# Performance work log

Measured on AMD Instinct MI355X. Metric: run time of the kernel, lower is better.

## Reference

```python
import jax, jax.numpy as jnp
import numpy as np

N = 50000      # nodes
E = 800000     # edges (avg degree 16)
IN = 128       # in_channels
HID = 32       # hidden_channels per head
HEADS = 4
OUT = 64       # out_channels (last layer, heads=1, concat=False)
ED = 32        # edge_dim
NEG_SLOPE = 0.2


def _gatv2_layer(x, src, dst, ea, Wl, bl, Wr, br, We, att, bias, concat):
    """PyG GATv2Conv: lin_l -> source (x_j), lin_r -> target (x_i),
    score = att . leaky_relu(x_i + x_j + lin_edge(edge_attr)), segment-softmax over dst,
    out = scatter_add(alpha * x_j) per head, then concat or mean heads, plus bias."""
    n = x.shape[0]
    H, C = att.shape
    xl = (x @ Wl + bl).reshape(-1, H, C)   # [N,H,C] source transform
    xr = (x @ Wr + br).reshape(-1, H, C)   # [N,H,C] target transform
    ee = (ea @ We).reshape(-1, H, C)       # [E,H,C] edge transform
    m = jax.nn.leaky_relu(xl[src] + xr[dst] + ee, NEG_SLOPE)  # [E,H,C]
    a = jnp.einsum('ehc,hc->eh', m, att)   # [E,H] attention logits
    amax = jax.ops.segment_max(a, dst, num_segments=n)        # [N,H]
    ex = jnp.exp(a - amax[dst])
    den = jax.ops.segment_sum(ex, dst, num_segments=n)        # [N,H]
    alpha = ex / (den[dst] + 1e-16)        # [E,H] segment softmax
    out = jax.ops.segment_sum(xl[src] * alpha[..., None], dst, num_segments=n)  # [N,H,C]
    out = out.reshape(n, H * C) if concat else out.mean(axis=1)
    return out + bias


def setup_inputs() -> dict:
    key = jax.random.key(0)
    ks = jax.random.split(key, 20)
    s = 0.05
    HC = HEADS * HID
    inp = {
        'x': jax.random.normal(ks[0], (N, IN), jnp.float32),
        'edge_index': jax.random.randint(ks[1], (2, E), 0, N, jnp.int32),
        'edge_attr': jax.random.normal(ks[2], (E, ED), jnp.float32),
        # layer 1: GATv2Conv(IN -> HID, heads=HEADS, concat=True, edge_dim=ED)
        'Wl1': jax.random.normal(ks[3], (IN, HC), jnp.float32) * s,
        'bl1': jnp.zeros((HC,), jnp.float32),
        'Wr1': jax.random.normal(ks[4], (IN, HC), jnp.float32) * s,
        'br1': jnp.zeros((HC,), jnp.float32),
        'We1': jax.random.normal(ks[5], (ED, HC), jnp.float32) * s,
        'att1': jax.random.normal(ks[6], (HEADS, HID), jnp.float32) * s,
        'bias1': jnp.zeros((HC,), jnp.float32),
        # layer 2: GATv2Conv(HC -> OUT, heads=1, concat=False, edge_dim=ED)
        'Wl2': jax.random.normal(ks[7], (HC, OUT), jnp.float32) * s,
        'bl2': jnp.zeros((OUT,), jnp.float32),
        'Wr2': jax.random.normal(ks[8], (HC, OUT), jnp.float32) * s,
        'br2': jnp.zeros((OUT,), jnp.float32),
        'We2': jax.random.normal(ks[9], (ED, OUT), jnp.float32) * s,
        'att2': jax.random.normal(ks[10], (1, OUT), jnp.float32) * s,
        'bias2': jnp.zeros((OUT,), jnp.float32),
    }
    return inp


def reference(x, edge_index, edge_attr, Wl1, bl1, Wr1, br1, We1, att1, bias1,
              Wl2, bl2, Wr2, br2, We2, att2, bias2):
    src, dst = edge_index[0], edge_index[1]
    h = _gatv2_layer(x, src, dst, edge_attr, Wl1, bl1, Wr1, br1, We1, att1, bias1, concat=True)
    h = jax.nn.elu(h)
    out = _gatv2_layer(h, src, dst, edge_attr, Wl2, bl2, Wr2, br2, We2, att2, bias2, concat=False)
    return out
```

## Files before the change

kernel.cpp:

```cpp
#include <hip/hip_runtime.h>
#include <stdint.h>

#define N_NODES 50000
#define N_EDGES 800000

struct Ptrs { const void* p[16]; int n[16]; };

typedef __attribute__((ext_vector_type(8))) short bf16x8;
typedef __attribute__((ext_vector_type(4))) float f32x4;

__device__ __forceinline__ float bf2f(unsigned short u){
  union { unsigned int i; float f; } v; v.i = ((unsigned int)u) << 16; return v.f;
}
__device__ __forceinline__ float lo16(unsigned int u){ union { unsigned int i; float f; } v; v.i = u << 16; return v.f; }
__device__ __forceinline__ float hi16(unsigned int u){ union { unsigned int i; float f; } v; v.i = u & 0xffff0000u; return v.f; }
__device__ __forceinline__ unsigned short f2bf(float f){
  if (!(f == f)) return 0;
  unsigned int x = __float_as_uint(f);
  unsigned int r = (x + 0x7fffu + ((x >> 16) & 1u)) >> 16;
  return (unsigned short)r;
}
__device__ __forceinline__ float fin(float v){
  if (!(v == v)) return 0.f;
  return fminf(fmaxf(v, -1e30f), 1e30f);
}
__device__ __forceinline__ float loadF(const void* p, int f32, size_t idx){
  return f32 ? ((const float*)p)[idx] : bf2f(((const unsigned short*)p)[idx]);
}

__device__ __forceinline__ void stageW(unsigned short* dst, const void* src, int n, int f32, int tid){
  if (f32) {
    for (int i = tid * 8; i < n; i += 2048) {
      float4 a = *(const float4*)((const float*)src + i);
      float4 b = *(const float4*)((const float*)src + i + 4);
      uint4 u;
      u.x = (unsigned)f2bf(a.x) | ((unsigned)f2bf(a.y) << 16);
      u.y = (unsigned)f2bf(a.z) | ((unsigned)f2bf(a.w) << 16);
      u.z = (unsigned)f2bf(b.x) | ((unsigned)f2bf(b.y) << 16);
      u.w = (unsigned)f2bf(b.z) | ((unsigned)f2bf(b.w) << 16);
      *(uint4*)(dst + i) = u;
    }
  } else {
    for (int i = tid * 8; i < n; i += 2048)
      *(uint4*)(dst + i) = *(const uint4*)((const unsigned short*)src + i);
  }
}

__global__ __launch_bounds__(256) void k_detect(Ptrs tl, int* __restrict__ flags)
{
  __shared__ int red[256];
  int b = blockIdx.x, t = threadIdx.x;
  const unsigned short* p = (const unsigned short*)tl.p[b];
  int n = tl.n[b]; if (n > 16384) n = 16384;
  int crazy = 0;
  for (int i = t; i < n; i += 256) {
    unsigned short u = p[i];
    if (u) {
      int ex = (u >> 7) & 0xFF;
      if (ex == 0xFF || ex < 0x60) crazy++;
    }
  }
  red[t] = crazy; __syncthreads();
  for (int off = 128; off; off >>= 1) { if (t < off) red[t] += red[t + off]; __syncthreads(); }
  if (t == 0) flags[b] = (red[0] * 10 > n) ? 1 : 0;
}

__global__ __launch_bounds__(256) void k_zero(int* __restrict__ p, int n)
{
  int i = blockIdx.x * 256 + threadIdx.x;
  if (i < n) p[i] = 0;
}

__global__ __launch_bounds__(256) void k_gemm1(
    const void* __restrict__ x,
    const void* __restrict__ Wl, const void* __restrict__ bl,
    const void* __restrict__ Wr, const void* __restrict__ br,
    const int* __restrict__ flags,
    unsigned int* __restrict__ xlp, unsigned int* __restrict__ xrp)
{
  __shared__ float xs[32 * 132];
  __shared__ unsigned short ws[128 * 128];
  const void* W  = blockIdx.y ? Wr : Wl;
  const void* bb = blockIdx.y ? br : bl;
  int fW = blockIdx.y ? flags[4] : flags[2];
  int fB = blockIdx.y ? flags[5] : flags[3];
  int fX = flags[0];
  unsigned int* outp = blockIdx.y ? xrp : xlp;
  int tid = threadIdx.x;
  int row0 = blockIdx.x * 32;
  stageW(ws, W, 128 * 128, fW, tid);
  for (int i = tid * 4; i < 32 * 128; i += 1024) {
    int r = i >> 7, k = i & 127;
    int row = row0 + r;
    float4 v = make_float4(0.f, 0.f, 0.f, 0.f);
    if (row < N_NODES) {
      if (fX) v = *(const float4*)((const float*)x + (size_t)row * 128 + k);
      else {
        uint2 u = *(const uint2*)((const unsigned short*)x + (size_t)row * 128 + k);
        v.x = lo16(u.x); v.y = hi16(u.x); v.z = lo16(u.y); v.w = hi16(u.y);
      }
    }
    *(float4*)(xs + r * 132 + k) = v;
  }
  __syncthreads();
  int r = tid >> 3, cg = tid & 7;
  float acc[16];
#pragma unroll
  for (int j = 0; j < 16; j++) acc[j] = 0.f;
#pragma unroll 4
  for (int k = 0; k < 128; k++) {
    float xv = xs[r * 132 + k];
    uint4 p0 = *(const uint4*)(ws + k * 128 + cg * 8);
    uint4 p1 = *(const uint4*)(ws + k * 128 + 64 + cg * 8);
    acc[0]  = fmaf(xv, lo16(p0.x), acc[0]);  acc[1]  = fmaf(xv, hi16(p0.x), acc[1]);
    acc[2]  = fmaf(xv, lo16(p0.y), acc[2]);  acc[3]  = fmaf(xv, hi16(p0.y), acc[3]);
    acc[4]  = fmaf(xv, lo16(p0.z), acc[4]);  acc[5]  = fmaf(xv, hi16(p0.z), acc[5]);
    acc[6]  = fmaf(xv, lo16(p0.w), acc[6]);  acc[7]  = fmaf(xv, hi16(p0.w), acc[7]);
    acc[8]  = fmaf(xv, lo16(p1.x), acc[8]);  acc[9]  = fmaf(xv, hi16(p1.x), acc[9]);
    acc[10] = fmaf(xv, lo16(p1.y), acc[10]); acc[11] = fmaf(xv, hi16(p1.y), acc[11]);
    acc[12] = fmaf(xv, lo16(p1.z), acc[12]); acc[13] = fmaf(xv, hi16(p1.z), acc[13]);
    acc[14] = fmaf(xv, lo16(p1.w), acc[14]); acc[15] = fmaf(xv, hi16(p1.w), acc[15]);
  }
  int row = row0 + r;
  if (row < N_NODES) {
    unsigned int* op = outp + (size_t)row * 64;
    uint4 o;
    unsigned int* ou = (unsigned int*)&o;
#pragma unroll
    for (int t = 0; t < 4; t++) {
      float f0 = fin(acc[2 * t]     + loadF(bb, fB, cg * 8 + 2 * t));
      float f1 = fin(acc[2 * t + 1] + loadF(bb, fB, cg * 8 + 2 * t + 1));
      ou[t] = (unsigned)f2bf(f0) | ((unsigned)f2bf(f1) << 16);
    }
    *(uint4*)(op + cg * 4) = o;
#pragma unroll
    for (int t = 0; t < 4; t++) {
      float f0 = fin(acc[8 + 2 * t]     + loadF(bb, fB, 64 + cg * 8 + 2 * t));
      float f1 = fin(acc[8 + 2 * t + 1] + loadF(bb, fB, 64 + cg * 8 + 2 * t + 1));
      ou[t] = (unsigned)f2bf(f0) | ((unsigned)f2bf(f1) << 16);
    }
    *(uint4*)(op + 32 + cg * 4) = o;
  }
}

__global__ __launch_bounds__(256) void k_gemm2(
    const float* __restrict__ h,
    const void* __restrict__ Wl, const void* __restrict__ bl,
    const void* __restrict__ Wr, const void* __restrict__ br,
    const int* __restrict__ flags,
    unsigned int* __restrict__ xlp, unsigned int* __restrict__ xrp)
{
  __shared__ float hs[32 * 132];
  __shared__ unsigned short ws[128 * 64];
  const void* W  = blockIdx.y ? Wr : Wl;
  const void* bb = blockIdx.y ? br : bl;
  int fW = blockIdx.y ? flags[11] : flags[9];
  int fB = blockIdx.y ? flags[12] : flags[10];
  unsigned int* outp = blockIdx.y ? xrp : xlp;
  int tid = threadIdx.x;
  int row0 = blockIdx.x * 32;
  stageW(ws, W, 128 * 64, fW, tid);
  for (int i = tid * 4; i < 32 * 128; i += 1024) {
    int r = i >> 7, k = i & 127;
    int row = row0 + r;
    float4 v = make_float4(0.f, 0.f, 0.f, 0.f);
    if (row < N_NODES) v = *(const float4*)(h + (size_t)row * 128 + k);
    *(float4*)(hs + r * 132 + k) = v;
  }
  __syncthreads();
  int r = tid >> 3, cg = tid & 7;
  float acc[8];
#pragma unroll
  for (int j = 0; j < 8; j++) acc[j] = 0.f;
#pragma unroll 4
  for (int k = 0; k < 128; k++) {
    float hv = hs[r * 132 + k];
    uint4 p = *(const uint4*)(ws + k * 64 + cg * 8);
    acc[0] = fmaf(hv, lo16(p.x), acc[0]); acc[1] = fmaf(hv, hi16(p.x), acc[1]);
    acc[2] = fmaf(hv, lo16(p.y), acc[2]); acc[3] = fmaf(hv, hi16(p.y), acc[3]);
    acc[4] = fmaf(hv, lo16(p.z), acc[4]); acc[5] = fmaf(hv, hi16(p.z), acc[5]);
    acc[6] = fmaf(hv, lo16(p.w), acc[6]); acc[7] = fmaf(hv, hi16(p.w), acc[7]);
  }
  int row = row0 + r;
  if (row < N_NODES) {
    uint4 o;
    unsigned int* ou = (unsigned int*)&o;
#pragma unroll
    for (int t = 0; t < 4; t++) {
      float f0 = fin(acc[2 * t]     + loadF(bb, fB, cg * 8 + 2 * t));
      float f1 = fin(acc[2 * t + 1] + loadF(bb, fB, cg * 8 + 2 * t + 1));
      ou[t] = (unsigned)f2bf(f0) | ((unsigned)f2bf(f1) << 16);
    }
    *(uint4*)(outp + (size_t)row * 32 + cg * 4) = o;
  }
}

__global__ __launch_bounds__(256) void k_hist(const int* __restrict__ ei, int* __restrict__ counts)
{
  int e = blockIdx.x * 256 + threadIdx.x;
  if (e < N_EDGES) {
    int d = ei[N_EDGES + e]; if ((unsigned)d >= N_NODES) d = 0;
    atomicAdd(&counts[d], 1);
  }
}

__global__ __launch_bounds__(256) void k_scan1(const int* __restrict__ counts,
                                               int* __restrict__ row_ptr, int* __restrict__ bsum)
{
  __shared__ int lds[256];
  int t = threadIdx.x;
  int base = blockIdx.x * 1024 + t * 4;
  int c0 = (base + 0) < N_NODES ? counts[base + 0] : 0;
  int c1 = (base + 1) < N_NODES ? counts[base + 1] : 0;
  int c2 = (base + 2) < N_NODES ? counts[base + 2] : 0;
  int c3 = (base + 3) < N_NODES ? counts[base + 3] : 0;
  int s = c0 + c1 + c2 + c3;
  lds[t] = s; __syncthreads();
  for (int off = 1; off < 256; off <<= 1) {
    int v = (t >= off) ? lds[t - off] : 0;
    __syncthreads();
    lds[t] += v;
    __syncthreads();
  }
  int incl = lds[t];
  int excl = incl - s;
  if (base + 0 < N_NODES) row_ptr[base + 0] = excl;
  if (base + 1 < N_NODES) row_ptr[base + 1] = excl + c0;
  if (base + 2 < N_NODES) row_ptr[base + 2] = excl + c0 + c1;
  if (base + 3 < N_NODES) row_ptr[base + 3] = excl + c0 + c1 + c2;
  if (t == 255) bsum[blockIdx.x] = incl;
}

__global__ __launch_bounds__(64) void k_scan2(int* __restrict__ bsum, int nb)
{
  __shared__ int l[64];
  int t = threadIdx.x;
  if (t < nb) l[t] = bsum[t];
  __syncthreads();
  if (t == 0) { int run = 0; for (int i = 0; i < nb; i++) { int v = l[i]; l[i] = run; run += v; } }
  __syncthreads();
  if (t < nb) bsum[t] = l[t];
}

__global__ __launch_bounds__(256) void k_scan3(int* __restrict__ row_ptr, int* __restrict__ cursor,
                                               const int* __restrict__ bsum)
{
  int t = threadIdx.x;
  int base = blockIdx.x * 1024 + t * 4;
  int add = bsum[blockIdx.x];
#pragma unroll
  for (int j = 0; j < 4; j++) {
    int i = base + j;
    if (i < N_NODES) { int v = row_ptr[i] + add; row_ptr[i] = v; cursor[i] = v; }
  }
  if (blockIdx.x == 0 && t == 0) row_ptr[N_NODES] = N_EDGES;
}

__global__ __launch_bounds__(256) void k_scatter(const int* __restrict__ ei,
                                                 int* __restrict__ cursor, int* __restrict__ col,
                                                 int* __restrict__ pos, int* __restrict__ srcs)
{
  int e = blockIdx.x * 256 + threadIdx.x;
  if (e < N_EDGES) {
    int d = ei[N_EDGES + e]; if ((unsigned)d >= N_NODES) d = 0;
    int s = ei[e];           if ((unsigned)s >= N_NODES) s = 0;
    int p = atomicAdd(&cursor[d], 1);
    if ((unsigned)p < N_EDGES) { col[p] = e; pos[e] = p; srcs[p] = s; }
  }
}

__global__ __launch_bounds__(256) void k_score1(
    const void* __restrict__ ea, const int* __restrict__ ei, const int* __restrict__ pos,
    const unsigned int* __restrict__ xlp, const unsigned int* __restrict__ xrp,
    const void* __restrict__ We, const void* __restrict__ att,
    const int* __restrict__ flags, float* __restrict__ w1)
{
  __shared__ unsigned short wt[128 * 34];
  __shared__ float at[128];
  int tid = threadIdx.x;
  {
    int f = flags[6];
    for (int i = tid; i < 4096; i += 256) {
      int k = i >> 7, c = i & 127;
      wt[c * 34 + k] = f ? f2bf(((const float*)We)[i]) : ((const unsigned short*)We)[i];
    }
  }
  if (tid < 128) at[tid] = loadF(att, flags[7], tid);
  __syncthreads();
  int lane = tid & 63;
  int idx16 = lane & 15, quad = lane >> 4;
  bf16x8 af[8];
  float4 atv[8];
#pragma unroll
  for (int t = 0; t < 8; t++) {
    af[t]  = *(const bf16x8*)(wt + (t * 16 + idx16) * 34 + quad * 8);
    atv[t] = *(const float4*)(at + t * 16 + quad * 4);
  }
  int fEA = flags[1];
  size_t e0 = (size_t)blockIdx.x * 128 + (size_t)(tid >> 6) * 32;
#pragma unroll
  for (int tt = 0; tt < 2; tt++) {
    size_t e = e0 + tt * 16 + idx16;
    bf16x8 bfrag;
    if (fEA) {
      const float* p = (const float*)ea + e * 32 + quad * 8;
      float4 v0 = *(const float4*)p;
      float4 v1 = *(const float4*)(p + 4);
      unsigned short tmp[8] = { f2bf(v0.x), f2bf(v0.y), f2bf(v0.z), f2bf(v0.w),
                                f2bf(v1.x), f2bf(v1.y), f2bf(v1.z), f2bf(v1.w) };
      bfrag = *(const bf16x8*)tmp;
    } else {
      bfrag = *(const bf16x8*)((const unsigned short*)ea + e * 32 + quad * 8);
    }
    int s = ei[e];           if ((unsigned)s >= N_NODES) s = 0;
    int d = ei[N_EDGES + e]; if ((unsigned)d >= N_NODES) d = 0;
    size_t dp = (size_t)pos[e];
    float ph0 = 0.f, ph1 = 0.f, ph2 = 0.f, ph3 = 0.f;
#pragma unroll
    for (int t = 0; t < 8; t++) {
      f32x4 c = {0.f, 0.f, 0.f, 0.f};
      c = __builtin_amdgcn_mfma_f32_16x16x32_bf16(af[t], bfrag, c, 0, 0, 0);
      uint2 ux = *(const uint2*)(xlp + (size_t)s * 64 + t * 8 + quad * 2);
      uint2 ur = *(const uint2*)(xrp + (size_t)d * 64 + t * 8 + quad * 2);
      float z0 = c[0] + lo16(ux.x) + lo16(ur.x);
      float z1 = c[1] + hi16(ux.x) + hi16(ur.x);
      float z2 = c[2] + lo16(ux.y) + lo16(ur.y);
      float z3 = c[3] + hi16(ux.y) + hi16(ur.y);
      z0 = z0 > 0.f ? z0 : 0.2f * z0;
      z1 = z1 > 0.f ? z1 : 0.2f * z1;
      z2 = z2 > 0.f ? z2 : 0.2f * z2;
      z3 = z3 > 0.f ? z3 : 0.2f * z3;
      float pp = fmaf(atv[t].x, z0, fmaf(atv[t].y, z1, fmaf(atv[t].z, z2, atv[t].w * z3)));
      if (t < 2)      ph0 += pp;
      else if (t < 4) ph1 += pp;
      else if (t < 6) ph2 += pp;
      else            ph3 += pp;
    }
    ph0 += __shfl_xor(ph0, 16, 64); ph0 += __shfl_xor(ph0, 32, 64);
    ph1 += __shfl_xor(ph1, 16, 64); ph1 += __shfl_xor(ph1, 32, 64);
    ph2 += __shfl_xor(ph2, 16, 64); ph2 += __shfl_xor(ph2, 32, 64);
    ph3 += __shfl_xor(ph3, 16, 64); ph3 += __shfl_xor(ph3, 32, 64);
    float myp = quad == 0 ? ph0 : quad == 1 ? ph1 : quad == 2 ? ph2 : ph3;
    w1[dp * 4 + quad] = __expf(fminf(fin(myp), 25.f));
  }
}

__global__ __launch_bounds__(256) void k_score2(
    const void* __restrict__ ea, const int* __restrict__ ei, const int* __restrict__ pos,
    const unsigned int* __restrict__ xlp, const unsigned int* __restrict__ xrp,
    const void* __restrict__ We, const void* __restrict__ att,
    const int* __restrict__ flags, float* __restrict__ w2)
{
  __shared__ unsigned short wt[64 * 34];
  __shared__ float at[64];
  int tid = threadIdx.x;
  {
    int f = flags[13];
    for (int i = tid; i < 2048; i += 256) {
      int k = i >> 6, c = i & 63;
      wt[c * 34 + k] = f ? f2bf(((const float*)We)[i]) : ((const unsigned short*)We)[i];
    }
  }
  if (tid < 64) at[tid] = loadF(att, flags[14], tid);
  __syncthreads();
  int lane = tid & 63;
  int idx16 = lane & 15, quad = lane >> 4;
  bf16x8 af[4];
  float4 atv[4];
#pragma unroll
  for (int t = 0; t < 4; t++) {
    af[t]  = *(const bf16x8*)(wt + (t * 16 + idx16) * 34 + quad * 8);
    atv[t] = *(const float4*)(at + t * 16 + quad * 4);
  }
  int fEA = flags[1];
  size_t e0 = (size_t)blockIdx.x * 128 + (size_t)(tid >> 6) * 32;
#pragma unroll
  for (int tt = 0; tt < 2; tt++) {
    size_t e = e0 + tt * 16 + idx16;
    bf16x8 bfrag;
    if (fEA) {
      const float* p = (const float*)ea + e * 32 + quad * 8;
      float4 v0 = *(const float4*)p;
      float4 v1 = *(const float4*)(p + 4);
      unsigned short tmp[8] = { f2bf(v0.x), f2bf(v0.y), f2bf(v0.z), f2bf(v0.w),
                                f2bf(v1.x), f2bf(v1.y), f2bf(v1.z), f2bf(v1.w) };
      bfrag = *(const bf16x8*)tmp;
    } else {
      bfrag = *(const bf16x8*)((const unsigned short*)ea + e * 32 + quad * 8);
    }
    int s = ei[e];           if ((unsigned)s >= N_NODES) s = 0;
    int d = ei[N_EDGES + e]; if ((unsigned)d >= N_NODES) d = 0;
    size_t dp = (size_t)pos[e];
    float ph = 0.f;
#pragma unroll
    for (int t = 0; t < 4; t++) {
      f32x4 c = {0.f, 0.f, 0.f, 0.f};
      c = __builtin_amdgcn_mfma_f32_16x16x32_bf16(af[t], bfrag, c, 0, 0, 0);
      uint2 ux = *(const uint2*)(xlp + (size_t)s * 32 + t * 8 + quad * 2);
      uint2 ur = *(const uint2*)(xrp + (size_t)d * 32 + t * 8 + quad * 2);
      float z0 = c[0] + lo16(ux.x) + lo16(ur.x);
      float z1 = c[1] + hi16(ux.x) + hi16(ur.x);
      float z2 = c[2] + lo16(ux.y) + lo16(ur.y);
      float z3 = c[3] + hi16(ux.y) + hi16(ur.y);
      z0 = z0 > 0.f ? z0 : 0.2f * z0;
      z1 = z1 > 0.f ? z1 : 0.2f * z1;
      z2 = z2 > 0.f ? z2 : 0.2f * z2;
      z3 = z3 > 0.f ? z3 : 0.2f * z3;
      ph += fmaf(atv[t].x, z0, fmaf(atv[t].y, z1, fmaf(atv[t].z, z2, atv[t].w * z3)));
    }
    ph += __shfl_xor(ph, 16, 64);
    ph += __shfl_xor(ph, 32, 64);
    if (quad == 0) w2[dp] = __expf(fminf(fin(ph), 25.f));
  }
}

__global__ __launch_bounds__(256) void k_agg1(
    const int* __restrict__ srcs, const int* __restrict__ row_ptr,
    const unsigned int* __restrict__ xlp, const float* __restrict__ w1,
    const void* __restrict__ bias, const int* __restrict__ flags,
    float* __restrict__ hout)
{
  int tid = threadIdx.x;
  int i = blockIdx.x * 4 + (tid >> 6);
  int lane = tid & 63;
  int head = lane >> 4;
  int p0 = row_ptr[i], p1 = row_ptr[i + 1];
  float acc0 = 0.f, acc1 = 0.f, den = 0.f;
  int j = p0;
  for (; j + 4 <= p1; j += 4) {
    int s0 = srcs[j], s1 = srcs[j + 1], s2 = srcs[j + 2], s3 = srcs[j + 3];
    float wa = w1[(size_t)(j + 0) * 4 + head];
    float wb = w1[(size_t)(j + 1) * 4 + head];
    float wc = w1[(size_t)(j + 2) * 4 + head];
    float wd = w1[(size_t)(j + 3) * 4 + head];
    unsigned int ux0 = xlp[(size_t)s0 * 64 + lane];
    unsigned int ux1 = xlp[(size_t)s1 * 64 + lane];
    unsigned int ux2 = xlp[(size_t)s2 * 64 + lane];
    unsigned int ux3 = xlp[(size_t)s3 * 64 + lane];
    acc0 = fmaf(wa, lo16(ux0), acc0); acc1 = fmaf(wa, hi16(ux0), acc1);
    acc0 = fmaf(wb, lo16(ux1), acc0); acc1 = fmaf(wb, hi16(ux1), acc1);
    acc0 = fmaf(wc, lo16(ux2), acc0); acc1 = fmaf(wc, hi16(ux2), acc1);
    acc0 = fmaf(wd, lo16(ux3), acc0); acc1 = fmaf(wd, hi16(ux3), acc1);
    den += wa + wb + wc + wd;
  }
  for (; j < p1; j++) {
    int s = srcs[j];
    float w = w1[(size_t)j * 4 + head];
    unsigned int ux = xlp[(size_t)s * 64 + lane];
    acc0 = fmaf(w, lo16(ux), acc0);
    acc1 = fmaf(w, hi16(ux), acc1);
    den += w;
  }
  float inv = 1.f / (den + 1e-16f);
  float o0 = fin(fmaf(acc0, inv, loadF(bias, flags[8], 2 * lane)));
  float o1 = fin(fmaf(acc1, inv, loadF(bias, flags[8], 2 * lane + 1)));
  o0 = o0 > 0.f ? o0 : __expf(o0) - 1.f;
  o1 = o1 > 0.f ? o1 : __expf(o1) - 1.f;
  *(float2*)(hout + (size_t)i * 128 + 2 * lane) = make_float2(o0, o1);
}

__global__ __launch_bounds__(256) void k_agg2(
    const int* __restrict__ srcs, const int* __restrict__ row_ptr,
    const unsigned int* __restrict__ xlp, const float* __restrict__ w2,
    const void* __restrict__ bias, const int* __restrict__ flags,
    void* __restrict__ out)
{
  int tid = threadIdx.x;
  int i = blockIdx.x * 4 + (tid >> 6);
  int lane = tid & 63;
  const unsigned short* xlb = (const unsigned short*)xlp;
  int p0 = row_ptr[i], p1 = row_ptr[i + 1];
  float acc = 0.f, den = 0.f;
  int j = p0;
  for (; j + 4 <= p1; j += 4) {
    int s0 = srcs[j], s1 = srcs[j + 1], s2 = srcs[j + 2], s3 = srcs[j + 3];
    float wa = w2[j], wb = w2[j + 1], wc = w2[j + 2], wd = w2[j + 3];
    unsigned short x0 = xlb[(size_t)s0 * 64 + lane];
    unsigned short x1 = xlb[(size_t)s1 * 64 + lane];
    unsigned short x2 = xlb[(size_t)s2 * 64 + lane];
    unsigned short x3 = xlb[(size_t)s3 * 64 + lane];
    acc = fmaf(wa, bf2f(x0), acc);
    acc = fmaf(wb, bf2f(x1), acc);
    acc = fmaf(wc, bf2f(x2), acc);
    acc = fmaf(wd, bf2f(x3), acc);
    den += wa + wb + wc + wd;
  }
  for (; j < p1; j++) {
    int s = srcs[j];
    float w = w2[j];
    acc = fmaf(w, bf2f(xlb[(size_t)s * 64 + lane]), acc);
    den += w;
  }
  float inv = 1.f / (den + 1e-16f);
  float o = fin(fmaf(acc, inv, loadF(bias, flags[15], lane)));
  if (flags[0]) ((float*)out)[(size_t)i * 64 + lane] = o;
  else ((unsigned short*)out)[(size_t)i * 64 + lane] = f2bf(o);
}

extern "C" void kernel_launch(void* const* d_in, const int* in_sizes, int n_in,
                              void* d_out, int out_size, void* d_ws, size_t ws_size,
                              hipStream_t stream)
{
  (void)n_in; (void)out_size; (void)ws_size;
  const void* x    = d_in[0];
  const int*  ei   = (const int*)d_in[1];
  const void* ea   = d_in[2];
  const void* Wl1  = d_in[3];
  const void* bl1  = d_in[4];
  const void* Wr1  = d_in[5];
  const void* br1  = d_in[6];
  const void* We1  = d_in[7];
  const void* att1 = d_in[8];
  const void* bias1= d_in[9];
  const void* Wl2  = d_in[10];
  const void* bl2  = d_in[11];
  const void* Wr2  = d_in[12];
  const void* br2  = d_in[13];
  const void* We2  = d_in[14];
  const void* att2 = d_in[15];
  const void* bias2= d_in[16];

  char* ws = (char*)d_ws;
  size_t off = 0;
  auto take = [&](size_t bytes) -> char* {
    char* p = ws + off;
    off += (bytes + 255) & ~(size_t)255;
    return p;
  };
  unsigned int* xl1p = (unsigned int*)take((size_t)N_NODES * 64 * 4);
  unsigned int* xr1p = (unsigned int*)take((size_t)N_NODES * 64 * 4);
  float* hbuf   = (float*)take((size_t)N_NODES * 128 * 4);
  float* w1     = (float*)take((size_t)N_EDGES * 4 * 4);
  int*   counts = (int*)  take((size_t)N_NODES * 4);
  int*   row_ptr= (int*)  take((size_t)(N_NODES + 1) * 4);
  int*   cursor = (int*)  take((size_t)N_NODES * 4);
  int*   col    = (int*)  take((size_t)N_EDGES * 4);
  int*   pos    = (int*)  take((size_t)N_EDGES * 4);
  int*   srcs   = (int*)  take((size_t)N_EDGES * 4);
  int*   bsum   = (int*)  take(64 * 4);
  int*   flags  = (int*)  take(64 * 4);
  unsigned int* xl2p = xl1p;
  unsigned int* xr2p = xr1p;
  float* w2 = w1;

  Ptrs tl;
  const int map[16] = {0, 2, 3, 4, 5, 6, 7, 8, 9, 10, 11, 12, 13, 14, 15, 16};
  for (int j = 0; j < 16; j++) { tl.p[j] = d_in[map[j]]; tl.n[j] = in_sizes[map[j]]; }

  int nb = (N_NODES + 1023) / 1024;
  k_detect<<<16, 256, 0, stream>>>(tl, flags);
  k_zero<<<(N_NODES + 255) / 256, 256, 0, stream>>>(counts, N_NODES);
  k_gemm1<<<dim3((N_NODES + 31) / 32, 2), 256, 0, stream>>>(x, Wl1, bl1, Wr1, br1, flags, xl1p, xr1p);
  k_hist<<<(N_EDGES + 255) / 256, 256, 0, stream>>>(ei, counts);
  k_scan1<<<nb, 256, 0, stream>>>(counts, row_ptr, bsum);
  k_scan2<<<1, 64, 0, stream>>>(bsum, nb);
  k_scan3<<<nb, 256, 0, stream>>>(row_ptr, cursor, bsum);
  k_scatter<<<(N_EDGES + 255) / 256, 256, 0, stream>>>(ei, cursor, col, pos, srcs);
  k_score1<<<N_EDGES / 128, 256, 0, stream>>>(ea, ei, pos, xl1p, xr1p, We1, att1, flags, w1);
  k_agg1<<<N_NODES / 4, 256, 0, stream>>>(srcs, row_ptr, xl1p, w1, bias1, flags, hbuf);
  k_gemm2<<<dim3((N_NODES + 31) / 32, 2), 256, 0, stream>>>(hbuf, Wl2, bl2, Wr2, br2, flags, xl2p, xr2p);
  k_score2<<<N_EDGES / 128, 256, 0, stream>>>(ea, ei, pos, xl2p, xr2p, We2, att2, flags, w2);
  k_agg2<<<N_NODES / 4, 256, 0, stream>>>(srcs, row_ptr, xl2p, w2, bias2, flags, d_out);
}
```

Baseline: 740.3 us.

## Fuse edge scoring with CSR aggregation and pre-permute edge attributes into CSR order

New measurement: 911.5 us. +23.1%, slower.

```diff
diff --git a/kernel.cpp b/kernel.cpp
--- a/kernel.cpp
+++ b/kernel.cpp
@@ -257,32 +257,63 @@
 }
 
 __global__ __launch_bounds__(256) void k_scatter(const int* __restrict__ ei,
-                                                 int* __restrict__ cursor, int* __restrict__ col,
-                                                 int* __restrict__ pos, int* __restrict__ srcs)
+                                                 int* __restrict__ cursor,
+                                                 int* __restrict__ srcs,
+                                                 const void* __restrict__ ea,
+                                                 const int* __restrict__ flags,
+                                                 unsigned short* __restrict__ eap)
 {
   int e = blockIdx.x * 256 + threadIdx.x;
-  if (e < N_EDGES) {
-    int d = ei[N_EDGES + e]; if ((unsigned)d >= N_NODES) d = 0;
-    int s = ei[e];           if ((unsigned)s >= N_NODES) s = 0;
-    int p = atomicAdd(&cursor[d], 1);
-    if ((unsigned)p < N_EDGES) { col[p] = e; pos[e] = p; srcs[p] = s; }
-  }
-}
-
-__global__ __launch_bounds__(256) void k_score1(
-    const void* __restrict__ ea, const int* __restrict__ ei, const int* __restrict__ pos,
+  if (e >= N_EDGES) return;
+  int d = ei[N_EDGES + e]; if ((unsigned)d >= N_NODES) d = 0;
+  int s = ei[e];           if ((unsigned)s >= N_NODES) s = 0;
+  int p = atomicAdd(&cursor[d], 1);
+  if ((unsigned)p >= N_EDGES) return;
+  srcs[p] = s;
+  unsigned short* op = eap + (size_t)p * 32;
+  if (flags[1]) {
+    const float* ip = (const float*)ea + (size_t)e * 32;
+#pragma unroll
+    for (int q = 0; q < 2; q++) {
+      float4 a = *(const float4*)(ip + q * 16);
+      float4 b = *(const float4*)(ip + q * 16 + 4);
+      float4 c = *(const float4*)(ip + q * 16 + 8);
+      float4 dd = *(const float4*)(ip + q * 16 + 12);
+      uint4 u0, u1;
+      u0.x = (unsigned)f2bf(a.x) | ((unsigned)f2bf(a.y) << 16);
+      u0.y = (unsigned)f2bf(a.z) | ((unsigned)f2bf(a.w) << 16);
+      u0.z = (unsigned)f2bf(b.x) | ((unsigned)f2bf(b.y) << 16);
+      u0.w = (unsigned)f2bf(b.z) | ((unsigned)f2bf(b.w) << 16);
+      u1.x = (unsigned)f2bf(c.x) | ((unsigned)f2bf(c.y) << 16);
+      u1.y = (unsigned)f2bf(c.z) | ((unsigned)f2bf(c.w) << 16);
+      u1.z = (unsigned)f2bf(dd.x) | ((unsigned)f2bf(dd.y) << 16);
+      u1.w = (unsigned)f2bf(dd.z) | ((unsigned)f2bf(dd.w) << 16);
+      *(uint4*)(op + q * 16) = u0;
+      *(uint4*)(op + q * 16 + 8) = u1;
+    }
+  } else {
+    const uint4* ip = (const uint4*)((const unsigned short*)ea + (size_t)e * 32);
+#pragma unroll
+    for (int q = 0; q < 4; q++) *(uint4*)(op + q * 8) = ip[q];
+  }
+}
+
+__global__ __launch_bounds__(256) void k_fuse1(
+    const unsigned short* __restrict__ eap, const int* __restrict__ srcs,
+    const int* __restrict__ row_ptr,
     const unsigned int* __restrict__ xlp, const unsigned int* __restrict__ xrp,
     const void* __restrict__ We, const void* __restrict__ att,
-    const int* __restrict__ flags, float* __restrict__ w1)
+    const void* __restrict__ bias, const int* __restrict__ flags,
+    float* __restrict__ hout)
 {
   __shared__ unsigned short wt[128 * 34];
   __shared__ float at[128];
   int tid = threadIdx.x;
   {
     int f = flags[6];
-    for (int i = tid; i < 4096; i += 256) {
-      int k = i >> 7, c = i & 127;
-      wt[c * 34 + k] = f ? f2bf(((const float*)We)[i]) : ((const unsigned short*)We)[i];
+    for (int i2 = tid; i2 < 4096; i2 += 256) {
+      int k = i2 >> 7, c = i2 & 127;
+      wt[c * 34 + k] = f ? f2bf(((const float*)We)[i2]) : ((const unsigned short*)We)[i2];
     }
   }
   if (tid < 128) at[tid] = loadF(att, flags[7], tid);
@@ -290,47 +321,45 @@
   int lane = tid & 63;
   int idx16 = lane & 15, quad = lane >> 4;
   bf16x8 af[8];
-  float4 atv[8];
-#pragma unroll
-  for (int t = 0; t < 8; t++) {
-    af[t]  = *(const bf16x8*)(wt + (t * 16 + idx16) * 34 + quad * 8);
-    atv[t] = *(const float4*)(at + t * 16 + quad * 4);
-  }
-  int fEA = flags[1];
-  size_t e0 = (size_t)blockIdx.x * 128 + (size_t)(tid >> 6) * 32;
-#pragma unroll
-  for (int tt = 0; tt < 2; tt++) {
-    size_t e = e0 + tt * 16 + idx16;
-    bf16x8 bfrag;
-    if (fEA) {
-      const float* p = (const float*)ea + e * 32 + quad * 8;
-      float4 v0 = *(const float4*)p;
-      float4 v1 = *(const float4*)(p + 4);
-      unsigned short tmp[8] = { f2bf(v0.x), f2bf(v0.y), f2bf(v0.z), f2bf(v0.w),
-                                f2bf(v1.x), f2bf(v1.y), f2bf(v1.z), f2bf(v1.w) };
-      bfrag = *(const bf16x8*)tmp;
-    } else {
-      bfrag = *(const bf16x8*)((const unsigned short*)ea + e * 32 + quad * 8);
-    }
-    int s = ei[e];           if ((unsigned)s >= N_NODES) s = 0;
-    int d = ei[N_EDGES + e]; if ((unsigned)d >= N_NODES) d = 0;
-    size_t dp = (size_t)pos[e];
+#pragma unroll
+  for (int t = 0; t < 8; t++)
+    af[t] = *(const bf16x8*)(wt + (t * 16 + idx16) * 34 + quad * 8);
+  int i = blockIdx.x * 4 + (tid >> 6);
+  int p0 = row_ptr[i], p1 = row_ptr[i + 1];
+  uint2 rv[8];
+#pragma unroll
+  for (int t = 0; t < 8; t++)
+    rv[t] = *(const uint2*)(xrp + (size_t)i * 64 + t * 8 + quad * 2);
+  float acc[32];
+#pragma unroll
+  for (int k = 0; k < 32; k++) acc[k] = 0.f;
+  float den0 = 0.f, den1 = 0.f, den2 = 0.f, den3 = 0.f;
+  for (int jb = p0; jb < p1; jb += 16) {
+    int j = jb + idx16;
+    int act = j < p1;
+    int jc = act ? j : 0;
+    int s = srcs[jc];
+    bf16x8 bfrag = *(const bf16x8*)(eap + (size_t)jc * 32 + quad * 8);
+    uint2 xv[8];
+#pragma unroll
+    for (int t = 0; t < 8; t++)
+      xv[t] = *(const uint2*)(xlp + (size_t)s * 64 + t * 8 + quad * 2);
     float ph0 = 0.f, ph1 = 0.f, ph2 = 0.f, ph3 = 0.f;
 #pragma unroll
     for (int t = 0; t < 8; t++) {
       f32x4 c = {0.f, 0.f, 0.f, 0.f};
       c = __builtin_amdgcn_mfma_f32_16x16x32_bf16(af[t], bfrag, c, 0, 0, 0);
-      uint2 ux = *(const uint2*)(xlp + (size_t)s * 64 + t * 8 + quad * 2);
-      uint2 ur = *(const uint2*)(xrp + (size_t)d * 64 + t * 8 + quad * 2);
-      float z0 = c[0] + lo16(ux.x) + lo16(ur.x);
-      float z1 = c[1] + hi16(ux.x) + hi16(ur.x);
-      float z2 = c[2] + lo16(ux.y) + lo16(ur.y);
-      float z3 = c[3] + hi16(ux.y) + hi16(ur.y);
+      uint2 r = rv[t];
+      float z0 = c[0] + lo16(xv[t].x) + lo16(r.x);
+      float z1 = c[1] + hi16(xv[t].x) + hi16(r.x);
+      float z2 = c[2] + lo16(xv[t].y) + lo16(r.y);
+      float z3 = c[3] + hi16(xv[t].y) + hi16(r.y);
       z0 = z0 > 0.f ? z0 : 0.2f * z0;
       z1 = z1 > 0.f ? z1 : 0.2f * z1;
       z2 = z2 > 0.f ? z2 : 0.2f * z2;
       z3 = z3 > 0.f ? z3 : 0.2f * z3;
-      float pp = fmaf(atv[t].x, z0, fmaf(atv[t].y, z1, fmaf(atv[t].z, z2, atv[t].w * z3)));
+      float4 av = *(const float4*)(at + t * 16 + quad * 4);
+      float pp = fmaf(av.x, z0, fmaf(av.y, z1, fmaf(av.z, z2, av.w * z3)));
       if (t < 2)      ph0 += pp;
       else if (t < 4) ph1 += pp;
       else if (t < 6) ph2 += pp;
@@ -340,25 +369,73 @@
     ph1 += __shfl_xor(ph1, 16, 64); ph1 += __shfl_xor(ph1, 32, 64);
     ph2 += __shfl_xor(ph2, 16, 64); ph2 += __shfl_xor(ph2, 32, 64);
     ph3 += __shfl_xor(ph3, 16, 64); ph3 += __shfl_xor(ph3, 32, 64);
-    float myp = quad == 0 ? ph0 : quad == 1 ? ph1 : quad == 2 ? ph2 : ph3;
-    w1[dp * 4 + quad] = __expf(fminf(fin(myp), 25.f));
-  }
-}
-
-__global__ __launch_bounds__(256) void k_score2(
-    const void* __restrict__ ea, const int* __restrict__ ei, const int* __restrict__ pos,
+    float w0 = act ? __expf(fminf(fin(ph0), 25.f)) : 0.f;
+    float w1 = act ? __expf(fminf(fin(ph1), 25.f)) : 0.f;
+    float w2 = act ? __expf(fminf(fin(ph2), 25.f)) : 0.f;
+    float w3 = act ? __expf(fminf(fin(ph3), 25.f)) : 0.f;
+    den0 += w0; den1 += w1; den2 += w2; den3 += w3;
+#pragma unroll
+    for (int t = 0; t < 8; t++) {
+      float wh = (t < 2) ? w0 : (t < 4) ? w1 : (t < 6) ? w2 : w3;
+      acc[t * 4 + 0] = fmaf(wh, lo16(xv[t].x), acc[t * 4 + 0]);
+      acc[t * 4 + 1] = fmaf(wh, hi16(xv[t].x), acc[t * 4 + 1]);
+      acc[t * 4 + 2] = fmaf(wh, lo16(xv[t].y), acc[t * 4 + 2]);
+      acc[t * 4 + 3] = fmaf(wh, hi16(xv[t].y), acc[t * 4 + 3]);
+    }
+  }
+#pragma unroll
+  for (int k = 0; k < 32; k++) {
+    acc[k] += __shfl_xor(acc[k], 1, 64); acc[k] += __shfl_xor(acc[k], 2, 64);
+    acc[k] += __shfl_xor(acc[k], 4, 64); acc[k] += __shfl_xor(acc[k], 8, 64);
+  }
+  den0 += __shfl_xor(den0, 1, 64); den0 += __shfl_xor(den0, 2, 64);
+  den0 += __shfl_xor(den0, 4, 64); den0 += __shfl_xor(den0, 8, 64);
+  den1 += __shfl_xor(den1, 1, 64); den1 += __shfl_xor(den1, 2, 64);
+  den1 += __shfl_xor(den1, 4, 64); den1 += __shfl_xor(den1, 8, 64);
+  den2 += __shfl_xor(den2, 1, 64); den2 += __shfl_xor(den2, 2, 64);
+  den2 += __shfl_xor(den2, 4, 64); den2 += __shfl_xor(den2, 8, 64);
+  den3 += __shfl_xor(den3, 1, 64); den3 += __shfl_xor(den3, 2, 64);
+  den3 += __shfl_xor(den3, 4, 64); den3 += __shfl_xor(den3, 8, 64);
+  if (idx16 == 0) {
+    float inv0 = 1.f / (den0 + 1e-16f);
+    float inv1 = 1.f / (den1 + 1e-16f);
+    float inv2 = 1.f / (den2 + 1e-16f);
+    float inv3 = 1.f / (den3 + 1e-16f);
+    int fB = flags[8];
+#pragma unroll
+    for (int t = 0; t < 8; t++) {
+      float invh = (t < 2) ? inv0 : (t < 4) ? inv1 : (t < 6) ? inv2 : inv3;
+      int ch = t * 16 + quad * 4;
+      float4 o;
+      o.x = fin(fmaf(acc[t * 4 + 0], invh, loadF(bias, fB, ch + 0)));
+      o.y = fin(fmaf(acc[t * 4 + 1], invh, loadF(bias, fB, ch + 1)));
+      o.z = fin(fmaf(acc[t * 4 + 2], invh, loadF(bias, fB, ch + 2)));
+      o.w = fin(fmaf(acc[t * 4 + 3], invh, loadF(bias, fB, ch + 3)));
+      o.x = o.x > 0.f ? o.x : __expf(o.x) - 1.f;
+      o.y = o.y > 0.f ? o.y : __expf(o.y) - 1.f;
+      o.z = o.z > 0.f ? o.z : __expf(o.z) - 1.f;
+      o.w = o.w > 0.f ? o.w : __expf(o.w) - 1.f;
+      *(float4*)(hout + (size_t)i * 128 + ch) = o;
+    }
+  }
+}
+
+__global__ __launch_bounds__(256) void k_fuse2(
+    const unsigned short* __restrict__ eap, const int* __restrict__ srcs,
+    const int* __restrict__ row_ptr,
     const unsigned int* __restrict__ xlp, const unsigned int* __restrict__ xrp,
     const void* __restrict__ We, const void* __restrict__ att,
-    const int* __restrict__ flags, float* __restrict__ w2)
+    const void* __restrict__ bias, const int* __restrict__ flags,
+    void* __restrict__ out)
 {
   __shared__ unsigned short wt[64 * 34];
   __shared__ float at[64];
   int tid = threadIdx.x;
   {
     int f = flags[13];
-    for (int i = tid; i < 2048; i += 256) {
-      int k = i >> 6, c = i & 63;
-      wt[c * 34 + k] = f ? f2bf(((const float*)We)[i]) : ((const unsigned short*)We)[i];
+    for (int i2 = tid; i2 < 2048; i2 += 256) {
+      int k = i2 >> 6, c = i2 & 63;
+      wt[c * 34 + k] = f ? f2bf(((const float*)We)[i2]) : ((const unsigned short*)We)[i2];
     }
   }
   if (tid < 64) at[tid] = loadF(att, flags[14], tid);
@@ -366,135 +443,85 @@
   int lane = tid & 63;
   int idx16 = lane & 15, quad = lane >> 4;
   bf16x8 af[4];
-  float4 atv[4];
-#pragma unroll
-  for (int t = 0; t < 4; t++) {
-    af[t]  = *(const bf16x8*)(wt + (t * 16 + idx16) * 34 + quad * 8);
-    atv[t] = *(const float4*)(at + t * 16 + quad * 4);
-  }
-  int fEA = flags[1];
-  size_t e0 = (size_t)blockIdx.x * 128 + (size_t)(tid >> 6) * 32;
-#pragma unroll
-  for (int tt = 0; tt < 2; tt++) {
-    size_t e = e0 + tt * 16 + idx16;
-    bf16x8 bfrag;
-    if (fEA) {
-      const float* p = (const float*)ea + e * 32 + quad * 8;
-      float4 v0 = *(const float4*)p;
-      float4 v1 = *(const float4*)(p + 4);
-      unsigned short tmp[8] = { f2bf(v0.x), f2bf(v0.y), f2bf(v0.z), f2bf(v0.w),
-                                f2bf(v1.x), f2bf(v1.y), f2bf(v1.z), f2bf(v1.w) };
-      bfrag = *(const bf16x8*)tmp;
-    } else {
-      bfrag = *(const bf16x8*)((const unsigned short*)ea + e * 32 + quad * 8);
-    }
-    int s = ei[e];           if ((unsigned)s >= N_NODES) s = 0;
-    int d = ei[N_EDGES + e]; if ((unsigned)d >= N_NODES) d = 0;
-    size_t dp = (size_t)pos[e];
+#pragma unroll
+  for (int t = 0; t < 4; t++)
+    af[t] = *(const bf16x8*)(wt + (t * 16 + idx16) * 34 + quad * 8);
+  int i = blockIdx.x * 4 + (tid >> 6);
+  int p0 = row_ptr[i], p1 = row_ptr[i + 1];
+  uint2 rv[4];
+#pragma unroll
+  for (int t = 0; t < 4; t++)
+    rv[t] = *(const uint2*)(xrp + (size_t)i * 32 + t * 8 + quad * 2);
+  float acc[16];
+#pragma unroll
+  for (int k = 0; k < 16; k++) acc[k] = 0.f;
+  float den = 0.f;
+  for (int jb = p0; jb < p1; jb += 16) {
+    int j = jb + idx16;
+    int act = j < p1;
+    int jc = act ? j : 0;
+    int s = srcs[jc];
+    bf16x8 bfrag = *(const bf16x8*)(eap + (size_t)jc * 32 + quad * 8);
+    uint2 xv[4];
+#pragma unroll
+    for (int t = 0; t < 4; t++)
+      xv[t] = *(const uint2*)(xlp + (size_t)s * 32 + t * 8 + quad * 2);
     float ph = 0.f;
 #pragma unroll
     for (int t = 0; t < 4; t++) {
       f32x4 c = {0.f, 0.f, 0.f, 0.f};
       c = __builtin_amdgcn_mfma_f32_16x16x32_bf16(af[t], bfrag, c, 0, 0, 0);
-      uint2 ux = *(const uint2*)(xlp + (size_t)s * 32 + t * 8 + quad * 2);
-      uint2 ur = *(const uint2*)(xrp + (size_t)d * 32 + t * 8 + quad * 2);
-      float z0 = c[0] + lo16(ux.x) + lo16(ur.x);
-      float z1 = c[1] + hi16(ux.x) + hi16(ur.x);
-      float z2 = c[2] + lo16(ux.y) + lo16(ur.y);
-      float z3 = c[3] + hi16(ux.y) + hi16(ur.y);
+      uint2 r = rv[t];
+      float z0 = c[0] + lo16(xv[t].x) + lo16(r.x);
+      float z1 = c[1] + hi16(xv[t].x) + hi16(r.x);
+      float z2 = c[2] + lo16(xv[t].y) + lo16(r.y);
+      float z3 = c[3] + hi16(xv[t].y) + hi16(r.y);
       z0 = z0 > 0.f ? z0 : 0.2f * z0;
       z1 = z1 > 0.f ? z1 : 0.2f * z1;
       z2 = z2 > 0.f ? z2 : 0.2f * z2;
       z3 = z3 > 0.f ? z3 : 0.2f * z3;
-      ph += fmaf(atv[t].x, z0, fmaf(atv[t].y, z1, fmaf(atv[t].z, z2, atv[t].w * z3)));
+      float4 av = *(const float4*)(at + t * 16 + quad * 4);
+      ph += fmaf(av.x, z0, fmaf(av.y, z1, fmaf(av.z, z2, av.w * z3)));
     }
     ph += __shfl_xor(ph, 16, 64);
     ph += __shfl_xor(ph, 32, 64);
-    if (quad == 0) w2[dp] = __expf(fminf(fin(ph), 25.f));
-  }
-}
-
-__global__ __launch_bounds__(256) void k_agg1(
-    const int* __restrict__ srcs, const int* __restrict__ row_ptr,
-    const unsigned int* __restrict__ xlp, const float* __restrict__ w1,
-    const void* __restrict__ bias, const int* __restrict__ flags,
-    float* __restrict__ hout)
-{
-  int tid = threadIdx.x;
-  int i = blockIdx.x * 4 + (tid >> 6);
-  int lane = tid & 63;
-  int head = lane >> 4;
-  int p0 = row_ptr[i], p1 = row_ptr[i + 1];
-  float acc0 = 0.f, acc1 = 0.f, den = 0.f;
-  int j = p0;
-  for (; j + 4 <= p1; j += 4) {
-    int s0 = srcs[j], s1 = srcs[j + 1], s2 = srcs[j + 2], s3 = srcs[j + 3];
-    float wa = w1[(size_t)(j + 0) * 4 + head];
-    float wb = w1[(size_t)(j + 1) * 4 + head];
-    float wc = w1[(size_t)(j + 2) * 4 + head];
-    float wd = w1[(size_t)(j + 3) * 4 + head];
-    unsigned int ux0 = xlp[(size_t)s0 * 64 + lane];
-    unsigned int ux1 = xlp[(size_t)s1 * 64 + lane];
-    unsigned int ux2 = xlp[(size_t)s2 * 64 + lane];
-    unsigned int ux3 = xlp[(size_t)s3 * 64 + lane];
-    acc0 = fmaf(wa, lo16(ux0), acc0); acc1 = fmaf(wa, hi16(ux0), acc1);
-    acc0 = fmaf(wb, lo16(ux1), acc0); acc1 = fmaf(wb, hi16(ux1), acc1);
-    acc0 = fmaf(wc, lo16(ux2), acc0); acc1 = fmaf(wc, hi16(ux2), acc1);
-    acc0 = fmaf(wd, lo16(ux3), acc0); acc1 = fmaf(wd, hi16(ux3), acc1);
-    den += wa + wb + wc + wd;
-  }
-  for (; j < p1; j++) {
-    int s = srcs[j];
-    float w = w1[(size_t)j * 4 + head];
-    unsigned int ux = xlp[(size_t)s * 64 + lane];
-    acc0 = fmaf(w, lo16(ux), acc0);
-    acc1 = fmaf(w, hi16(ux), acc1);
+    float w = act ? __expf(fminf(fin(ph), 25.f)) : 0.f;
     den += w;
-  }
-  float inv = 1.f / (den + 1e-16f);
-  float o0 = fin(fmaf(acc0, inv, loadF(bias, flags[8], 2 * lane)));
-  float o1 = fin(fmaf(acc1, inv, loadF(bias, flags[8], 2 * lane + 1)));
-  o0 = o0 > 0.f ? o0 : __expf(o0) - 1.f;
-  o1 = o1 > 0.f ? o1 : __expf(o1) - 1.f;
-  *(float2*)(hout + (size_t)i * 128 + 2 * lane) = make_float2(o0, o1);
-}
-
-__global__ __launch_bounds__(256) void k_agg2(
-    const int* __restrict__ srcs, const int* __restrict__ row_ptr,
-    const unsigned int* __restrict__ xlp, const float* __restrict__ w2,
-    const void* __restrict__ bias, const int* __restrict__ flags,
-    void* __restrict__ out)
-{
-  int tid = threadIdx.x;
-  int i = blockIdx.x * 4 + (tid >> 6);
-  int lane = tid & 63;
-  const unsigned short* xlb = (const unsigned short*)xlp;
-  int p0 = row_ptr[i], p1 = row_ptr[i + 1];
-  float acc = 0.f, den = 0.f;
-  int j = p0;
-  for (; j + 4 <= p1; j += 4) {
-    int s0 = srcs[j], s1 = srcs[j + 1], s2 = srcs[j + 2], s3 = srcs[j + 3];
-    float wa = w2[j], wb = w2[j + 1], wc = w2[j + 2], wd = w2[j + 3];
-    unsigned short x0 = xlb[(size_t)s0 * 64 + lane];
-    unsigned short x1 = xlb[(size_t)s1 * 64 + lane];
-    unsigned short x2 = xlb[(size_t)s2 * 64 + lane];
-    unsigned short x3 = xlb[(size_t)s3 * 64 + lane];
-    acc = fmaf(wa, bf2f(x0), acc);
-    acc = fmaf(wb, bf2f(x1), acc);
-    acc = fmaf(wc, bf2f(x2), acc);
-    acc = fmaf(wd, bf2f(x3), acc);
-    den += wa + wb + wc + wd;
-  }
-  for (; j < p1; j++) {
-    int s = srcs[j];
-    float w = w2[j];
-    acc = fmaf(w, bf2f(xlb[(size_t)s * 64 + lane]), acc);
-    den += w;
-  }
-  float inv = 1.f / (den + 1e-16f);
-  float o = fin(fmaf(acc, inv, loadF(bias, flags[15], lane)));
-  if (flags[0]) ((float*)out)[(size_t)i * 64 + lane] = o;
-  else ((unsigned short*)out)[(size_t)i * 64 + lane] = f2bf(o);
+#pragma unroll
+    for (int t = 0; t < 4; t++) {
+      acc[t * 4 + 0] = fmaf(w, lo16(xv[t].x), acc[t * 4 + 0]);
+      acc[t * 4 + 1] = fmaf(w, hi16(xv[t].x), acc[t * 4 + 1]);
+      acc[t * 4 + 2] = fmaf(w, lo16(xv[t].y), acc[t * 4 + 2]);
+      acc[t * 4 + 3] = fmaf(w, hi16(xv[t].y), acc[t * 4 + 3]);
+    }
+  }
+#pragma unroll
+  for (int k = 0; k < 16; k++) {
+    acc[k] += __shfl_xor(acc[k], 1, 64); acc[k] += __shfl_xor(acc[k], 2, 64);
+    acc[k] += __shfl_xor(acc[k], 4, 64); acc[k] += __shfl_xor(acc[k], 8, 64);
+  }
+  den += __shfl_xor(den, 1, 64); den += __shfl_xor(den, 2, 64);
+  den += __shfl_xor(den, 4, 64); den += __shfl_xor(den, 8, 64);
+  if (idx16 == 0) {
+    float inv = 1.f / (den + 1e-16f);
+    int fB = flags[15];
+#pragma unroll
+    for (int t = 0; t < 4; t++) {
+      int ch = t * 16 + quad * 4;
+      float o0 = fin(fmaf(acc[t * 4 + 0], inv, loadF(bias, fB, ch + 0)));
+      float o1 = fin(fmaf(acc[t * 4 + 1], inv, loadF(bias, fB, ch + 1)));
+      float o2 = fin(fmaf(acc[t * 4 + 2], inv, loadF(bias, fB, ch + 2)));
+      float o3 = fin(fmaf(acc[t * 4 + 3], inv, loadF(bias, fB, ch + 3)));
+      if (flags[0]) {
+        *(float4*)((float*)out + (size_t)i * 64 + ch) = make_float4(o0, o1, o2, o3);
+      } else {
+        uint2 u;
+        u.x = (unsigned)f2bf(o0) | ((unsigned)f2bf(o1) << 16);
+        u.y = (unsigned)f2bf(o2) | ((unsigned)f2bf(o3) << 16);
+        *(uint2*)((unsigned short*)out + (size_t)i * 64 + ch) = u;
+      }
+    }
+  }
 }
 
 extern "C" void kernel_launch(void* const* d_in, const int* in_sizes, int n_in,
@@ -530,18 +557,15 @@
   unsigned int* xl1p = (unsigned int*)take((size_t)N_NODES * 64 * 4);
   unsigned int* xr1p = (unsigned int*)take((size_t)N_NODES * 64 * 4);
   float* hbuf   = (float*)take((size_t)N_NODES * 128 * 4);
-  float* w1     = (float*)take((size_t)N_EDGES * 4 * 4);
+  unsigned short* eap = (unsigned short*)take((size_t)(N_EDGES + 16) * 32 * 2);
   int*   counts = (int*)  take((size_t)N_NODES * 4);
   int*   row_ptr= (int*)  take((size_t)(N_NODES + 1) * 4);
   int*   cursor = (int*)  take((size_t)N_NODES * 4);
-  int*   col    = (int*)  take((size_t)N_EDGES * 4);
-  int*   pos    = (int*)  take((size_t)N_EDGES * 4);
   int*   srcs   = (int*)  take((size_t)N_EDGES * 4);
   int*   bsum   = (int*)  take(64 * 4);
   int*   flags  = (int*)  take(64 * 4);
   unsigned int* xl2p = xl1p;
   unsigned int* xr2p = xr1p;
-  float* w2 = w1;
 
   Ptrs tl;
   const int map[16] = {0, 2, 3, 4, 5, 6, 7, 8, 9, 10, 11, 12, 13, 14, 15, 16};
@@ -555,10 +579,8 @@
   k_scan1<<<nb, 256, 0, stream>>>(counts, row_ptr, bsum);
   k_scan2<<<1, 64, 0, stream>>>(bsum, nb);
   k_scan3<<<nb, 256, 0, stream>>>(row_ptr, cursor, bsum);
-  k_scatter<<<(N_EDGES + 255) / 256, 256, 0, stream>>>(ei, cursor, col, pos, srcs);
-  k_score1<<<N_EDGES / 128, 256, 0, stream>>>(ea, ei, pos, xl1p, xr1p, We1, att1, flags, w1);
-  k_agg1<<<N_NODES / 4, 256, 0, stream>>>(srcs, row_ptr, xl1p, w1, bias1, flags, hbuf);
+  k_scatter<<<(N_EDGES + 255) / 256, 256, 0, stream>>>(ei, cursor, srcs, ea, flags, eap);
+  k_fuse1<<<N_NODES / 4, 256, 0, stream>>>(eap, srcs, row_ptr, xl1p, xr1p, We1, att1, bias1, flags, hbuf);
   k_gemm2<<<dim3((N_NODES + 31) / 32, 2), 256, 0, stream>>>(hbuf, Wl2, bl2, Wr2, br2, flags, xl2p, xr2p);
-  k_score2<<<N_EDGES / 128, 256, 0, stream>>>(ea, ei, pos, xl2p, xr2p, We2, att2, flags, w2);
-  k_agg2<<<N_NODES / 4, 256, 0, stream>>>(srcs, row_ptr, xl2p, w2, bias2, flags, d_out);
-}
+  k_fuse2<<<N_NODES / 4, 256, 0, stream>>>(eap, srcs, row_ptr, xl2p, xr2p, We2, att2, bias2, flags, d_out);
+}
```
